# Kernel optimization log

Measured on AMD Instinct MI355X. Metric: run time of the kernel, lower is better.

## Reference

```python
import jax, jax.numpy as jnp
import numpy as np

B = 262144          # batch of sample points
L = 16              # hash levels
T = 1 << 19         # hash table size per level
F = 2               # features per level
BASE_RES = 16
FINEST_RES = 512
DH = 64             # density MLP hidden
DOUT = 16           # density MLP out (density_out dim)
CH = 64             # color MLP hidden
PRIMES = np.array([1, 2654435761, 805459861], dtype=np.uint32)
_b = np.exp((np.log(FINEST_RES) - np.log(BASE_RES)) / (L - 1))
RES = jnp.asarray(np.floor(BASE_RES * _b ** np.arange(L)).astype(np.float32))  # (L,)


def _linear_init(key, fan_in, fan_out):
    kw, kb = jax.random.split(key)
    bound = 1.0 / np.sqrt(fan_in)
    w = jax.random.uniform(kw, (fan_in, fan_out), minval=-bound, maxval=bound)
    b = jax.random.uniform(kb, (fan_out,), minval=-bound, maxval=bound)
    return w, b


def setup_inputs() -> dict:
    key = jax.random.key(0)
    ks = jax.random.split(key, 10)
    coords = jax.random.uniform(ks[0], (B, 3), dtype=jnp.float32)          # in [0,1]
    directions = jax.random.normal(ks[1], (B, 3), dtype=jnp.float32)
    embeddings = jax.random.uniform(ks[2], (L, T, F), minval=-1e-4, maxval=1e-4, dtype=jnp.float32)
    dw1, db1 = _linear_init(ks[3], L * F, DH)
    dw2, db2 = _linear_init(ks[4], DH, DOUT)
    cw1, cb1 = _linear_init(ks[5], 16 + DOUT, CH)
    cw2, cb2 = _linear_init(ks[6], CH, CH)
    cw3, cb3 = _linear_init(ks[7], CH, CH)
    cw4, cb4 = _linear_init(ks[8], CH, 3)
    return dict(coords=coords, directions=directions, embeddings=embeddings,
                dw1=dw1, db1=db1, dw2=dw2, db2=db2,
                cw1=cw1, cb1=cb1, cw2=cw2, cb2=cb2,
                cw3=cw3, cb3=cb3, cw4=cw4, cb4=cb4)


def hash_encode(coords, embeddings):
    # coords: (B,3) in [0,1]; embeddings: (L,T,F)
    pos = coords[:, None, :] * RES[None, :, None]            # (B,L,3)
    p0 = jnp.floor(pos)
    frac = pos - p0                                           # (B,L,3)
    p0 = p0.astype(jnp.uint32)
    corners = jnp.stack([p0, p0 + jnp.uint32(1)], axis=-1)    # (B,L,3,2)
    h_ax = corners * jnp.asarray(PRIMES)[None, None, :, None]  # uint32 wraparound
    hidx = (h_ax[:, :, 0, :, None, None]
            ^ h_ax[:, :, 1, None, :, None]
            ^ h_ax[:, :, 2, None, None, :])                   # (B,L,2,2,2)
    hidx = (hidx & jnp.uint32(T - 1)).reshape(coords.shape[0], L, 8).astype(jnp.int32)
    feats = embeddings[jnp.arange(L)[None, :, None], hidx]    # (B,L,8,F)
    wx = jnp.stack([1.0 - frac[..., 0], frac[..., 0]], -1)    # (B,L,2)
    wy = jnp.stack([1.0 - frac[..., 1], frac[..., 1]], -1)
    wz = jnp.stack([1.0 - frac[..., 2], frac[..., 2]], -1)
    w = (wx[:, :, :, None, None] * wy[:, :, None, :, None] * wz[:, :, None, None, :])
    w = w.reshape(coords.shape[0], L, 8)                      # (B,L,8)
    out = jnp.sum(feats * w[..., None], axis=2)               # (B,L,F)
    return out.reshape(coords.shape[0], L * F)


def sh_encode_deg4(d):
    # d: (B,3) unit directions in [-1,1]; degree-4 real SH basis (16 comps)
    x, y, z = d[:, 0], d[:, 1], d[:, 2]
    xx, yy, zz = x * x, y * y, z * z
    xy, yz, xz = x * y, y * z, x * z
    c = jnp.full_like(x, 0.28209479177387814)
    return jnp.stack([
        c,
        -0.48860251190291987 * y,
        0.48860251190291987 * z,
        -0.48860251190291987 * x,
        1.0925484305920792 * xy,
        -1.0925484305920792 * yz,
        0.94617469575755997 * zz - 0.31539156525251999,
        -1.0925484305920792 * xz,
        0.54627421529603959 * (xx - yy),
        0.59004358992664352 * y * (-3.0 * xx + yy),
        2.8906114426405538 * xy * z,
        0.45704579946446572 * y * (1.0 - 5.0 * zz),
        0.3731763325901154 * z * (5.0 * zz - 3.0),
        0.45704579946446572 * x * (1.0 - 5.0 * zz),
        1.4453057213202769 * z * (xx - yy),
        0.59004358992664352 * x * (xx - 3.0 * yy),
    ], axis=1)


def reference(coords, directions, embeddings, dw1, db1, dw2, db2,
              cw1, cb1, cw2, cb2, cw3, cb3, cw4, cb4):
    # density net: hash encode -> Linear+ReLU -> Linear
    feat = hash_encode(coords, embeddings)                    # (B, L*F)
    h = jax.nn.relu(feat @ dw1 + db1)
    density_out = h @ dw2 + db2                               # (B, DOUT)
    density = jnp.exp(density_out[:, 0])                      # TruncExp fwd = exp
    # color net
    d = directions / jnp.linalg.norm(directions, axis=1, keepdims=True)
    d01 = (d + 1.0) / 2.0                                     # remap as in module
    sh = sh_encode_deg4(d01 * 2.0 - 1.0)                      # encoder maps back to [-1,1]
    inp = jnp.concatenate([sh, density_out], axis=1)          # (B, 32)
    x = jax.nn.relu(inp @ cw1 + cb1)
    x = jax.nn.relu(x @ cw2 + cb2)
    x = jax.nn.relu(x @ cw3 + cb3)
    color = jax.nn.sigmoid(x @ cw4 + cb4)                     # (B, 3)
    return density, color
```

## Files before the change

kernel.cpp:

```cpp
#include <hip/hip_runtime.h>
#include <cmath>

#define NPTS 262144
#define NLVL 16
#define TBL  524288u
#define TMASK 524287u
#define TPB  256
#define NQ   7

typedef __attribute__((ext_vector_type(8))) short short8;
typedef __attribute__((ext_vector_type(4))) float f32x4;

struct ResArr { float r[NLVL]; };
struct QuadInfo { int off[NQ]; int dim[NQ]; };

__device__ __forceinline__ unsigned short f2bf(float f) {
    union { float f; unsigned u; } v; v.f = f;
    unsigned r = v.u + 0x7FFFu + ((v.u >> 16) & 1u);
    return (unsigned short)(r >> 16);
}
__device__ __forceinline__ float blo(unsigned u) {
    union { unsigned v; float f; } x; x.v = u << 16; return x.f;
}
__device__ __forceinline__ float bhi(unsigned u) {
    union { unsigned v; float f; } x; x.v = u & 0xffff0000u; return x.f;
}
__device__ __forceinline__ unsigned packbf(float a, float b) {
    return (unsigned)f2bf(a) | ((unsigned)f2bf(b) << 16);
}

#define MFMA(a,b,c) __builtin_amdgcn_mfma_f32_16x16x32_bf16((a),(b),(c),0,0,0)

__global__ __launch_bounds__(256) void fused_encode_k(
    const float* __restrict__ coords,
    const float* __restrict__ emb,
    uint4* __restrict__ oct,
    unsigned* __restrict__ featws,
    const float* __restrict__ dw1, const float* __restrict__ db1,
    const float* __restrict__ dw2, const float* __restrict__ db2,
    const float* __restrict__ cw1, const float* __restrict__ cb1,
    const float* __restrict__ cw2, const float* __restrict__ cb2,
    const float* __restrict__ cw3, const float* __restrict__ cb3,
    const float* __restrict__ cw4, const float* __restrict__ cb4,
    unsigned short* __restrict__ wpk, float* __restrict__ bpk,
    ResArr res, QuadInfo qi, int ncell, int ncb, int tailn)
{
    const int tid = threadIdx.x;
    const int b   = blockIdx.x;
    const int xcd = b & 7;
    const int s   = b >> 3;

    if (s < 1152) {
        int l, p;
        if (s < 1024) {
            l = 7 + xcd;
            p = s * 256 + tid;
        } else {
            l = 15;
            p = xcd * 32768 + (s - 1024) * 256 + tid;
        }

        const float cx = coords[3*p], cy = coords[3*p+1], cz = coords[3*p+2];
        const float r = res.r[l];
        const float px = cx*r, py = cy*r, pz = cz*r;
        const float fpx = floorf(px), fpy = floorf(py), fpz = floorf(pz);
        const float fx = px-fpx, fy = py-fpy, fz = pz-fpz;
        const unsigned ix=(unsigned)fpx, iy=(unsigned)fpy, iz=(unsigned)fpz;
        const unsigned hy0=iy*2654435761u, hy1=(iy+1u)*2654435761u;
        const unsigned hz0=iz*805459861u,  hz1=(iz+1u)*805459861u;
        const unsigned base  = (unsigned)l * TBL;
        const unsigned base4 = (unsigned)l * (TBL >> 1);
        const float2* __restrict__ emb2 = (const float2*)emb;
        const float4* __restrict__ emb4 = (const float4*)emb;

        const unsigned m = ix ^ (ix + 1u);
        const unsigned h00 = (ix^hy0^hz0) & TMASK;
        const unsigned h01 = (ix^hy0^hz1) & TMASK;
        const unsigned h10 = (ix^hy1^hz0) & TMASK;
        const unsigned h11 = (ix^hy1^hz1) & TMASK;

        const float4 p00 = emb4[base4 + (h00 >> 1)];
        const float4 p01 = emb4[base4 + (h01 >> 1)];
        const float4 p10 = emb4[base4 + (h10 >> 1)];
        const float4 p11 = emb4[base4 + (h11 >> 1)];

        float2 f000, f001, f010, f011, f100, f101, f110, f111;
        f000.x = (h00&1) ? p00.z : p00.x;  f000.y = (h00&1) ? p00.w : p00.y;
        f001.x = (h01&1) ? p01.z : p01.x;  f001.y = (h01&1) ? p01.w : p01.y;
        f010.x = (h10&1) ? p10.z : p10.x;  f010.y = (h10&1) ? p10.w : p10.y;
        f011.x = (h11&1) ? p11.z : p11.x;  f011.y = (h11&1) ? p11.w : p11.y;
        f100.x = (h00&1) ? p00.x : p00.z;  f100.y = (h00&1) ? p00.y : p00.w;
        f101.x = (h01&1) ? p01.x : p01.z;  f101.y = (h01&1) ? p01.y : p01.w;
        f110.x = (h10&1) ? p10.x : p10.z;  f110.y = (h10&1) ? p10.y : p10.w;
        f111.x = (h11&1) ? p11.x : p11.z;  f111.y = (h11&1) ? p11.y : p11.w;

        if (m != 1u) {
            f100 = emb2[base + ((h00 ^ m) & TMASK)];
            f101 = emb2[base + ((h01 ^ m) & TMASK)];
            f110 = emb2[base + ((h10 ^ m) & TMASK)];
            f111 = emb2[base + ((h11 ^ m) & TMASK)];
        }

        const float wx0=1.f-fx, wy0=1.f-fy, wz0=1.f-fz;
        float o0, o1;
        o0 = wx0*wy0*wz0*f000.x;                 o1 = wx0*wy0*wz0*f000.y;
        o0 = fmaf(wx0*wy0*fz,  f001.x, o0);      o1 = fmaf(wx0*wy0*fz,  f001.y, o1);
        o0 = fmaf(wx0*fy*wz0,  f010.x, o0);      o1 = fmaf(wx0*fy*wz0,  f010.y, o1);
        o0 = fmaf(wx0*fy*fz,   f011.x, o0);      o1 = fmaf(wx0*fy*fz,   f011.y, o1);
        o0 = fmaf(fx*wy0*wz0,  f100.x, o0);      o1 = fmaf(fx*wy0*wz0,  f100.y, o1);
        o0 = fmaf(fx*wy0*fz,   f101.x, o0);      o1 = fmaf(fx*wy0*fz,   f101.y, o1);
        o0 = fmaf(fx*fy*wz0,   f110.x, o0);      o1 = fmaf(fx*fy*wz0,   f110.y, o1);
        o0 = fmaf(fx*fy*fz,    f111.x, o0);      o1 = fmaf(fx*fy*fz,    f111.y, o1);

        featws[(size_t)l * NPTS + p] = packbf(o0, o1);
    } else {
        const int rank = xcd * tailn + (s - 1152);
        if (rank < ncb) {
            const int gcell = rank * 256 + tid;
            if (gcell >= ncell) return;

            int l = 0;
            #pragma unroll
            for (int j = 1; j < NQ; ++j) if (gcell >= qi.off[j]) l = j;
            const int off = qi.off[l];
            const int D   = qi.dim[l];
            const int t   = gcell - off;
            const int DD  = D*D;

            const unsigned z = (unsigned)t % (unsigned)D;
            const unsigned rem = (unsigned)t / (unsigned)D;
            const unsigned y = rem % (unsigned)D;
            const unsigned x = rem / (unsigned)D;

            const float2* __restrict__ emb2 = (const float2*)emb;
            const unsigned base = (unsigned)l * TBL;
            const unsigned hy0 = y*2654435761u, hy1 = (y+1u)*2654435761u;
            const unsigned hz0 = z*805459861u,  hz1 = (z+1u)*805459861u;

            const float2 a = emb2[base + ((x^hy0^hz0)&TMASK)];
            const float2 bb= emb2[base + ((x^hy0^hz1)&TMASK)];
            const float2 c = emb2[base + ((x^hy1^hz0)&TMASK)];
            const float2 d = emb2[base + ((x^hy1^hz1)&TMASK)];

            uint4 q;
            q.x = packbf(a.x, a.y);
            q.y = packbf(bb.x, bb.y);
            q.z = packbf(c.x, c.y);
            q.w = packbf(d.x, d.y);

            const int e = off + t;
            oct[2*e] = q;
            if (t >= DD)
                oct[2*(e - DD) + 1] = q;
        } else if (rank == ncb) {
            const int wid  = tid >> 6;
            const int lane = tid & 63;
            const int m16  = lane & 15;
            const int q    = lane >> 4;
            const unsigned char MAT[28] = {0,0,0,0, 1,1, 2,2,2,2, 3,3,3,3,3,3,3,3, 4,4,4,4,4,4,4,4, 5,5};
            const unsigned char K0 [28] = {0,0,0,0, 0,32, 0,0,0,0, 0,0,0,0,32,32,32,32, 0,0,0,0,32,32,32,32, 0,32};
            const unsigned char N0 [28] = {0,16,32,48, 0,0, 0,16,32,48, 0,16,32,48,0,16,32,48, 0,16,32,48,0,16,32,48, 0,0};
            #pragma unroll
            for (int s2 = 0; s2 < 28; ++s2) {
                if ((s2 & 3) == wid) {
                    const int mat = MAT[s2];
                    const float* src = mat==0?dw1 : mat==1?dw2 : mat==2?cw1 : mat==3?cw2 : mat==4?cw3 : cw4;
                    const int fan = (mat==1) ? 16 : (mat==5) ? 3 : 64;
                    const int k = (int)K0[s2] + q*8;
                    const int n = (int)N0[s2] + m16;
                    unsigned short u[8];
                    #pragma unroll
                    for (int j = 0; j < 8; ++j) {
                        float v = 0.f;
                        if (mat != 5 || n < 3) v = src[(k+j)*fan + n];
                        u[j] = f2bf(v);
                    }
                    unsigned* w32 = (unsigned*)(wpk + s2*512 + lane*8);
                    w32[0] = (unsigned)u[0] | ((unsigned)u[1] << 16);
                    w32[1] = (unsigned)u[2] | ((unsigned)u[3] << 16);
                    w32[2] = (unsigned)u[4] | ((unsigned)u[5] << 16);
                    w32[3] = (unsigned)u[6] | ((unsigned)u[7] << 16);
                }
            }
            {
                int t = tid;
                if      (t <  64) bpk[t] = db1[t];
                else if (t <  80) bpk[t] = db2[t-64];
                else if (t < 144) bpk[t] = cb1[t-80];
                else if (t < 208) bpk[t] = cb2[t-144];
            }
            if (tid < 80) {
                int t = tid + 208;
                if (t < 272) bpk[t] = cb3[t-208];
                else         bpk[t] = (t-272 < 3) ? cb4[t-272] : 0.f;
            }
        }
    }
}

__global__ __launch_bounds__(256, 3) void mlp_mfma_k(
    const unsigned* __restrict__ featws,
    const uint4* __restrict__ oct,
    const float* __restrict__ coords,
    const unsigned short* __restrict__ wpk,
    const float* __restrict__ bpk,
    const float* __restrict__ dirs,
    float* __restrict__ out,
    ResArr res, QuadInfo qi)
{
    const int tid  = threadIdx.x;
    const int wid  = tid >> 6;
    const int lane = tid & 63;
    const int m16  = lane & 15;
    const int q    = lane >> 4;

    __shared__ __align__(16) unsigned short wlds[28 * 512];
    __shared__ float blds[288];
    __shared__ __align__(16) unsigned short actL[4 * 16 * 72];
    __shared__ unsigned featO[256 * 8];

    {
        uint4* dst = (uint4*)wlds;
        const uint4* srcv = (const uint4*)wpk;
        #pragma unroll
        for (int j = 0; j < 7; ++j) dst[j*256 + tid] = srcv[j*256 + tid];
        if (tid < 256) blds[tid] = bpk[tid];
        if (tid < 32)  blds[256 + tid] = bpk[256 + tid];
    }

    const int pbase = blockIdx.x * TPB;

    {
        const int p = pbase + tid;
        const float cx = coords[3*p], cy = coords[3*p+1], cz = coords[3*p+2];
        #pragma unroll
        for (int l = 0; l < NQ; ++l) {
            const float r = res.r[l];
            const float px = cx*r, py = cy*r, pz = cz*r;
            const float fpx = floorf(px), fpy = floorf(py), fpz = floorf(pz);
            const float fx = px-fpx, fy = py-fpy, fz = pz-fpz;
            const int ix=(int)fpx, iy=(int)fpy, iz=(int)fpz;
            const int D = qi.dim[l];
            const int v0 = qi.off[l] + (ix*D + iy)*D + iz;
            const uint4 qA = oct[2*v0];
            const uint4 qB = oct[2*v0 + 1];
            const float wx0=1.f-fx, wy0=1.f-fy, wz0=1.f-fz;
            const float w000=wx0*wy0*wz0, w001=wx0*wy0*fz;
            const float w010=wx0*fy*wz0,  w011=wx0*fy*fz;
            const float w100=fx*wy0*wz0,  w101=fx*wy0*fz;
            const float w110=fx*fy*wz0,   w111=fx*fy*fz;
            float o0, o1;
            o0 = w000*blo(qA.x);              o1 = w000*bhi(qA.x);
            o0 = fmaf(w001, blo(qA.y), o0);   o1 = fmaf(w001, bhi(qA.y), o1);
            o0 = fmaf(w010, blo(qA.z), o0);   o1 = fmaf(w010, bhi(qA.z), o1);
            o0 = fmaf(w011, blo(qA.w), o0);   o1 = fmaf(w011, bhi(qA.w), o1);
            o0 = fmaf(w100, blo(qB.x), o0);   o1 = fmaf(w100, bhi(qB.x), o1);
            o0 = fmaf(w101, blo(qB.y), o0);   o1 = fmaf(w101, bhi(qB.y), o1);
            o0 = fmaf(w110, blo(qB.z), o0);   o1 = fmaf(w110, bhi(qB.z), o1);
            o0 = fmaf(w111, blo(qB.w), o0);   o1 = fmaf(w111, bhi(qB.w), o1);
            featO[tid*8 + l] = packbf(o0, o1);
        }
    }
    __syncthreads();

    unsigned short* aw = actL + wid*1152;
    const short8* wfr = (const short8*)wlds;

    #pragma unroll 1
    for (int iter = 0; iter < 4; ++iter) {
        const int tile = wid + 4*iter;
        const int loc0 = tile*16;
        const int p0g  = pbase + loc0;

        union { unsigned u[4]; short8 s; } af;
        #pragma unroll
        for (int j = 0; j < 4; ++j) {
            const int lvl = q*4 + j;
            af.u[j] = (lvl < NQ) ? featO[(loc0+m16)*8 + lvl]
                                 : featws[(size_t)lvl * NPTS + p0g + m16];
        }
        const short8 a0 = af.s;

        f32x4 acc[4];
        #pragma unroll
        for (int nc = 0; nc < 4; ++nc) {
            const float b = blds[nc*16 + m16];
            acc[nc] = (f32x4){b,b,b,b};
            acc[nc] = MFMA(a0, wfr[nc*64 + lane], acc[nc]);
        }
        #pragma unroll
        for (int nc = 0; nc < 4; ++nc)
            #pragma unroll
            for (int r = 0; r < 4; ++r)
                aw[(q*4+r)*72 + nc*16 + m16] = f2bf(fmaxf(acc[nc][r], 0.f));

        short8 ad0 = *(const short8*)(aw + m16*72 + q*8);
        short8 ad1 = *(const short8*)(aw + m16*72 + 32 + q*8);
        f32x4 dob;
        { const float b = blds[64 + m16]; dob = (f32x4){b,b,b,b}; }
        dob = MFMA(ad0, wfr[4*64 + lane], dob);
        dob = MFMA(ad1, wfr[5*64 + lane], dob);

        if (m16 == 0) {
            #pragma unroll
            for (int r = 0; r < 4; ++r) out[p0g + q*4 + r] = expf(dob[r]);
        }

        #pragma unroll
        for (int r = 0; r < 4; ++r)
            aw[(q*4+r)*72 + 16 + m16] = f2bf(dob[r]);
        {
            const int pg = p0g + m16;
            const float dx0 = dirs[3*pg], dy0 = dirs[3*pg+1], dz0 = dirs[3*pg+2];
            const float inv = 1.f / sqrtf(dx0*dx0 + dy0*dy0 + dz0*dz0);
            float x = dx0*inv, y = dy0*inv, z = dz0*inv;
            x = ((x+1.f)*0.5f)*2.f - 1.f;
            y = ((y+1.f)*0.5f)*2.f - 1.f;
            z = ((z+1.f)*0.5f)*2.f - 1.f;
            float s0, s1, s2, s3;
            switch (q) {
            case 0: s0 = 0.28209479177387814f;
                    s1 = -0.48860251190291987f*y;
                    s2 =  0.48860251190291987f*z;
                    s3 = -0.48860251190291987f*x; break;
            case 1: s0 =  1.0925484305920792f*x*y;
                    s1 = -1.0925484305920792f*y*z;
                    s2 =  0.94617469575756f*z*z - 0.31539156525252f;
                    s3 = -1.0925484305920792f*x*z; break;
            case 2: s0 =  0.5462742152960396f*(x*x - y*y);
                    s1 =  0.5900435899266435f*y*(-3.f*x*x + y*y);
                    s2 =  2.890611442640554f*x*y*z;
                    s3 =  0.4570457994644657f*y*(1.f - 5.f*z*z); break;
            default:s0 =  0.3731763325901154f*z*(5.f*z*z - 3.f);
                    s1 =  0.4570457994644657f*x*(1.f - 5.f*z*z);
                    s2 =  1.445305721320277f*z*(x*x - y*y);
                    s3 =  0.5900435899266435f*x*(x*x - 3.f*y*y); break;
            }
            unsigned* ip = (unsigned*)(aw + m16*72 + q*4);
            ip[0] = packbf(s0, s1);
            ip[1] = packbf(s2, s3);
        }

        short8 ac0 = *(const short8*)(aw + m16*72 + q*8);
        #pragma unroll
        for (int nc = 0; nc < 4; ++nc) {
            const float b = blds[80 + nc*16 + m16];
            acc[nc] = (f32x4){b,b,b,b};
            acc[nc] = MFMA(ac0, wfr[(6+nc)*64 + lane], acc[nc]);
        }
        #pragma unroll
        for (int nc = 0; nc < 4; ++nc)
            #pragma unroll
            for (int r = 0; r < 4; ++r)
                aw[(q*4+r)*72 + nc*16 + m16] = f2bf(fmaxf(acc[nc][r], 0.f));

        short8 a20 = *(const short8*)(aw + m16*72 + q*8);
        short8 a21 = *(const short8*)(aw + m16*72 + 32 + q*8);
        #pragma unroll
        for (int nc = 0; nc < 4; ++nc) {
            const float b = blds[144 + nc*16 + m16];
            acc[nc] = (f32x4){b,b,b,b};
            acc[nc] = MFMA(a20, wfr[(10+nc)*64 + lane], acc[nc]);
            acc[nc] = MFMA(a21, wfr[(14+nc)*64 + lane], acc[nc]);
        }
        #pragma unroll
        for (int nc = 0; nc < 4; ++nc)
            #pragma unroll
            for (int r = 0; r < 4; ++r)
                aw[(q*4+r)*72 + nc*16 + m16] = f2bf(fmaxf(acc[nc][r], 0.f));

        short8 a30 = *(const short8*)(aw + m16*72 + q*8);
        short8 a31 = *(const short8*)(aw + m16*72 + 32 + q*8);
        #pragma unroll
        for (int nc = 0; nc < 4; ++nc) {
            const float b = blds[208 + nc*16 + m16];
            acc[nc] = (f32x4){b,b,b,b};
            acc[nc] = MFMA(a30, wfr[(18+nc)*64 + lane], acc[nc]);
            acc[nc] = MFMA(a31, wfr[(22+nc)*64 + lane], acc[nc]);
        }
        #pragma unroll
        for (int nc = 0; nc < 4; ++nc)
            #pragma unroll
            for (int r = 0; r < 4; ++r)
                aw[(q*4+r)*72 + nc*16 + m16] = f2bf(fmaxf(acc[nc][r], 0.f));

        short8 a40 = *(const short8*)(aw + m16*72 + q*8);
        short8 a41 = *(const short8*)(aw + m16*72 + 32 + q*8);
        f32x4 c4v;
        { const float b = blds[272 + m16]; c4v = (f32x4){b,b,b,b}; }
        c4v = MFMA(a40, wfr[26*64 + lane], c4v);
        c4v = MFMA(a41, wfr[27*64 + lane], c4v);
        if (m16 < 3) {
            #pragma unroll
            for (int r = 0; r < 4; ++r)
                out[NPTS + 3*(p0g + q*4 + r) + m16] = 1.f / (1.f + expf(-c4v[r]));
        }
    }
}

extern "C" void kernel_launch(void* const* d_in, const int* in_sizes, int n_in,
                              void* d_out, int out_size, void* d_ws, size_t ws_size,
                              hipStream_t stream)
{
    ResArr res;
    const double b = exp((log(512.0) - log(16.0)) / 15.0);
    for (int l = 0; l < NLVL; ++l)
        res.r[l] = (float)floor(16.0 * pow(b, (double)l));

    QuadInfo qi;
    int ncell = 0;
    for (int l = 0; l < NQ; ++l) {
        const int D = (int)res.r[l] + 1;
        qi.dim[l] = D;
        qi.off[l] = ncell;
        ncell += D*D*D;
    }
    const int ncb   = (ncell + 255) / 256;
    const int tailn = (ncb + 1 + 7) / 8;
    const int smax  = 1152 + tailn;
    const int grid  = smax * 8;

    unsigned*       featws = (unsigned*)d_ws;
    uint4*          oct    = (uint4*)((char*)d_ws + (size_t)NLVL * NPTS * 4);
    unsigned short* wpk    = (unsigned short*)((char*)oct + (size_t)ncell * 32);
    float*          bpk    = (float*)((char*)wpk + 28 * 512 * 2);

    fused_encode_k<<<grid, 256, 0, stream>>>(
        (const float*)d_in[0],
        (const float*)d_in[2],
        oct, featws,
        (const float*)d_in[3],  (const float*)d_in[4],
        (const float*)d_in[5],  (const float*)d_in[6],
        (const float*)d_in[7],  (const float*)d_in[8],
        (const float*)d_in[9],  (const float*)d_in[10],
        (const float*)d_in[11], (const float*)d_in[12],
        (const float*)d_in[13], (const float*)d_in[14],
        wpk, bpk, res, qi, ncell, ncb, tailn);

    mlp_mfma_k<<<NPTS/TPB, 256, 0, stream>>>(
        featws, oct,
        (const float*)d_in[0],
        wpk, bpk,
        (const float*)d_in[1],
        (float*)d_out,
        res, qi);
}
```

Before: 229.6 us.

## Double block size and prefetch hashed features one tile ahead in MLP kernel

Grows the MLP kernel blocks to 512 threads (8 waves), so the LDS weight copy is amortized over twice as many points per block. It also software-pipelines the global loads of the workspace hash features: the first tile is loaded before the dense-grid interpolation, and each later tile's features are fetched during the current tile's MLP. The featO stride drops to 7 to save LDS. The trade-off is higher register pressure under launch_bounds(512,4) and possible occupancy changes from the larger LDS footprint.

```diff
diff --git a/kernel.cpp b/kernel.cpp
--- a/kernel.cpp
+++ b/kernel.cpp
@@ -5,7 +5,7 @@
 #define NLVL 16
 #define TBL  524288u
 #define TMASK 524287u
-#define TPB  256
+#define TPB  512
 #define NQ   7
 
 typedef __attribute__((ext_vector_type(8))) short short8;
@@ -198,7 +198,7 @@
     }
 }
 
-__global__ __launch_bounds__(256, 3) void mlp_mfma_k(
+__global__ __launch_bounds__(512, 4) void mlp_mfma_k(
     const unsigned* __restrict__ featws,
     const uint4* __restrict__ oct,
     const float* __restrict__ coords,
@@ -216,19 +216,31 @@
 
     __shared__ __align__(16) unsigned short wlds[28 * 512];
     __shared__ float blds[288];
-    __shared__ __align__(16) unsigned short actL[4 * 16 * 72];
-    __shared__ unsigned featO[256 * 8];
+    __shared__ __align__(16) unsigned short actL[8 * 16 * 72];
+    __shared__ unsigned featO[TPB * 7];
 
     {
         uint4* dst = (uint4*)wlds;
         const uint4* srcv = (const uint4*)wpk;
         #pragma unroll
-        for (int j = 0; j < 7; ++j) dst[j*256 + tid] = srcv[j*256 + tid];
-        if (tid < 256) blds[tid] = bpk[tid];
-        if (tid < 32)  blds[256 + tid] = bpk[256 + tid];
+        for (int j = 0; j < 4; ++j) {
+            const int idx = j*512 + tid;
+            if (idx < 1792) dst[idx] = srcv[idx];
+        }
+        if (tid < 288) blds[tid] = bpk[tid];
     }
 
     const int pbase = blockIdx.x * TPB;
+
+    unsigned g0, g1, g2, g3;
+    {
+        const int pg = pbase + wid*16 + m16;
+        const int l0 = q*4;
+        g0 = (l0+0 >= NQ) ? featws[(size_t)(l0+0) * NPTS + pg] : 0u;
+        g1 = (l0+1 >= NQ) ? featws[(size_t)(l0+1) * NPTS + pg] : 0u;
+        g2 = (l0+2 >= NQ) ? featws[(size_t)(l0+2) * NPTS + pg] : 0u;
+        g3 = (l0+3 >= NQ) ? featws[(size_t)(l0+3) * NPTS + pg] : 0u;
+    }
 
     {
         const int p = pbase + tid;
@@ -258,7 +270,7 @@
             o0 = fmaf(w101, blo(qB.y), o0);   o1 = fmaf(w101, bhi(qB.y), o1);
             o0 = fmaf(w110, blo(qB.z), o0);   o1 = fmaf(w110, bhi(qB.z), o1);
             o0 = fmaf(w111, blo(qB.w), o0);   o1 = fmaf(w111, bhi(qB.w), o1);
-            featO[tid*8 + l] = packbf(o0, o1);
+            featO[tid*7 + l] = packbf(o0, o1);
         }
     }
     __syncthreads();
@@ -268,16 +280,28 @@
 
     #pragma unroll 1
     for (int iter = 0; iter < 4; ++iter) {
-        const int tile = wid + 4*iter;
+        const int tile = wid + 8*iter;
         const int loc0 = tile*16;
         const int p0g  = pbase + loc0;
 
+        unsigned n0 = 0u, n1 = 0u, n2 = 0u, n3 = 0u;
+        if (iter < 3) {
+            const int pg = pbase + (wid + 8*(iter+1))*16 + m16;
+            const int l0 = q*4;
+            n0 = (l0+0 >= NQ) ? featws[(size_t)(l0+0) * NPTS + pg] : 0u;
+            n1 = (l0+1 >= NQ) ? featws[(size_t)(l0+1) * NPTS + pg] : 0u;
+            n2 = (l0+2 >= NQ) ? featws[(size_t)(l0+2) * NPTS + pg] : 0u;
+            n3 = (l0+3 >= NQ) ? featws[(size_t)(l0+3) * NPTS + pg] : 0u;
+        }
+
         union { unsigned u[4]; short8 s; } af;
-        #pragma unroll
-        for (int j = 0; j < 4; ++j) {
-            const int lvl = q*4 + j;
-            af.u[j] = (lvl < NQ) ? featO[(loc0+m16)*8 + lvl]
-                                 : featws[(size_t)lvl * NPTS + p0g + m16];
+        {
+            const int l0 = q*4;
+            const int rowb = (loc0 + m16) * 7;
+            af.u[0] = (l0+0 < NQ) ? featO[rowb + l0+0] : g0;
+            af.u[1] = (l0+1 < NQ) ? featO[rowb + l0+1] : g1;
+            af.u[2] = (l0+2 < NQ) ? featO[rowb + l0+2] : g2;
+            af.u[3] = (l0+3 < NQ) ? featO[rowb + l0+3] : g3;
         }
         const short8 a0 = af.s;
 
@@ -395,6 +419,8 @@
             for (int r = 0; r < 4; ++r)
                 out[NPTS + 3*(p0g + q*4 + r) + m16] = 1.f / (1.f + expf(-c4v[r]));
         }
+
+        g0 = n0; g1 = n1; g2 = n2; g3 = n3;
     }
 }
 
@@ -437,7 +463,7 @@
         (const float*)d_in[13], (const float*)d_in[14],
         wpk, bpk, res, qi, ncell, ncb, tailn);
 
-    mlp_mfma_k<<<NPTS/TPB, 256, 0, stream>>>(
+    mlp_mfma_k<<<NPTS/TPB, 512, 0, stream>>>(
         featws, oct,
         (const float*)d_in[0],
         wpk, bpk,
```

Result: no change. 226.0 us (-1.5%).
